# Optimization experiments

Hardware: AMD Instinct MI355X
Metric: run time of the kernel (lower is better)

## Reference

```python
import jax, jax.numpy as jnp
import numpy as np

GRID = 32  # hard-coded voxel resolution in the original module


def setup_inputs() -> dict:
    key = jax.random.key(0)
    k1, k2 = jax.random.split(key)
    points = jax.random.normal(k1, (4, 100000, 3), dtype=jnp.float32)
    features = jax.random.normal(k2, (4, 100000, 64), dtype=jnp.float32)
    return {"points": points, "features": features}


def reference(points, features):
    # points: [B, N, 3], features: [B, N, F]
    B, N, _ = points.shape
    Fdim = features.shape[-1]
    # Global (over whole tensor) min/max normalization, exactly as original
    pmin = points.min()
    pmax = points.max()
    normed = (points - pmin) / (pmax - pmin + 1e-6)  # in [0, 1)
    # torch: (normed // (1/32)).long() == floor(normed * 32)
    vox = jnp.floor(normed * GRID).astype(jnp.int32)  # [B, N, 3], values in [0, 31]
    gidx = vox[..., 0] * (GRID * GRID) + vox[..., 1] * GRID + vox[..., 2]  # [B, N]
    # Scatter-max into a zero-initialized grid (zeros init == implicit max with 0,
    # matching the original torch.zeros output_grid).
    grid = jnp.zeros((B, GRID ** 3, Fdim), dtype=features.dtype)
    batch_ids = jnp.arange(B, dtype=jnp.int32)[:, None]  # [B, 1] broadcast over N
    grid = grid.at[batch_ids, gidx].max(features)
    return grid.reshape(B, GRID, GRID, GRID, Fdim)
```

## Files before the change

### kernel.cpp

```cpp
#include <hip/hip_runtime.h>

#define GRID3 32768
#define FDIM 64

__device__ __forceinline__ unsigned int enc_f32(float f) {
    unsigned int u = __float_as_uint(f);
    return (u & 0x80000000u) ? ~u : (u | 0x80000000u);
}
__device__ __forceinline__ float dec_f32(unsigned int u) {
    u = (u & 0x80000000u) ? (u ^ 0x80000000u) : ~u;
    return __uint_as_float(u);
}

__global__ void init_ws_kernel(unsigned int* ws) {
    ws[0] = 0xFFFFFFFFu;
    ws[1] = 0u;
}

__global__ void minmax_kernel(const float* __restrict__ pts, int n,
                              unsigned int* __restrict__ ws) {
    float lmin = INFINITY, lmax = -INFINITY;
    for (int i = blockIdx.x * blockDim.x + threadIdx.x; i < n;
         i += gridDim.x * blockDim.x) {
        float v = pts[i];
        lmin = fminf(lmin, v);
        lmax = fmaxf(lmax, v);
    }
    __shared__ float smin[256], smax[256];
    smin[threadIdx.x] = lmin;
    smax[threadIdx.x] = lmax;
    __syncthreads();
    for (int s = 128; s > 0; s >>= 1) {
        if (threadIdx.x < (unsigned)s) {
            smin[threadIdx.x] = fminf(smin[threadIdx.x], smin[threadIdx.x + s]);
            smax[threadIdx.x] = fmaxf(smax[threadIdx.x], smax[threadIdx.x + s]);
        }
        __syncthreads();
    }
    if (threadIdx.x == 0) {
        atomicMin(&ws[0], enc_f32(smin[0]));
        atomicMax(&ws[1], enc_f32(smax[0]));
    }
}

__global__ void scatter_kernel(const float* __restrict__ pts,
                               const float* __restrict__ feat,
                               const unsigned int* __restrict__ ws,
                               unsigned int* __restrict__ out,
                               int ntot, int N) {
    int lane = threadIdx.x & 63;
    int p = blockIdx.x * 4 + (threadIdx.x >> 6);
    if (p >= ntot) return;

    float pmin = dec_f32(ws[0]);
    float pmax = dec_f32(ws[1]);
    float denom = pmax - pmin + 1e-6f;

    float x = pts[p * 3 + 0];
    float y = pts[p * 3 + 1];
    float z = pts[p * 3 + 2];

    int vx = (int)floorf(((x - pmin) / denom) * 32.0f);
    int vy = (int)floorf(((y - pmin) / denom) * 32.0f);
    int vz = (int)floorf(((z - pmin) / denom) * 32.0f);
    vx = min(max(vx, 0), 31);
    vy = min(max(vy, 0), 31);
    vz = min(max(vz, 0), 31);
    int gidx = vx * 1024 + vy * 32 + vz;

    int b = p / N;
    float f = feat[(size_t)p * FDIM + lane];

    if (f > 0.0f) {
        unsigned int* addr = out + ((size_t)b * GRID3 + gidx) * FDIM + lane;
        atomicMax(addr, __float_as_uint(f));
    }
}

extern "C" void kernel_launch(void* const* d_in, const int* in_sizes, int n_in,
                              void* d_out, int out_size, void* d_ws, size_t ws_size,
                              hipStream_t stream) {
    const float* pts = (const float*)d_in[0];
    const float* feat = (const float*)d_in[1];
    unsigned int* ws = (unsigned int*)d_ws;

    int npts3 = in_sizes[0];
    int ntot = npts3 / 3;
    int B = out_size / (GRID3 * FDIM);
    int N = ntot / B;

    hipLaunchKernelGGL(init_ws_kernel, dim3(1), dim3(1), 0, stream, ws);
    hipLaunchKernelGGL(minmax_kernel, dim3(512), dim3(256), 0, stream,
                       pts, npts3, ws);
    hipMemsetAsync(d_out, 0, (size_t)out_size * sizeof(float), stream);
    int blocks = (ntot + 3) / 4;
    hipLaunchKernelGGL(scatter_kernel, dim3(blocks), dim3(256), 0, stream,
                       pts, feat, ws, (unsigned int*)d_out, ntot, N);
}
```

Before: 250.7 us.

## Fuse zero-fill, min/max reduction and scatter into one cooperative kernel

```diff
diff --git a/kernel.cpp b/kernel.cpp
--- a/kernel.cpp
+++ b/kernel.cpp
@@ -1,79 +1,114 @@
 #include <hip/hip_runtime.h>
+#include <hip/hip_cooperative_groups.h>
+
+namespace cg = cooperative_groups;
 
 #define GRID3 32768
 #define FDIM 64
+#define NBLOCKS 1024
+#define NTHREADS 256
+#define MMBLOCKS 512
 
-__device__ __forceinline__ unsigned int enc_f32(float f) {
-    unsigned int u = __float_as_uint(f);
-    return (u & 0x80000000u) ? ~u : (u | 0x80000000u);
-}
-__device__ __forceinline__ float dec_f32(unsigned int u) {
-    u = (u & 0x80000000u) ? (u ^ 0x80000000u) : ~u;
-    return __uint_as_float(u);
-}
+__global__ __launch_bounds__(NTHREADS, 4)
+void fused_gridpool(const float* __restrict__ pts,
+                    const float* __restrict__ feat,
+                    unsigned int* __restrict__ out,
+                    float2* __restrict__ partials,
+                    int npts_floats,
+                    int ntot,
+                    int N,
+                    int out_floats)
+{
+    const int tid = threadIdx.x;
+    const int bid = blockIdx.x;
+    __shared__ float smin[NTHREADS];
+    __shared__ float smax[NTHREADS];
 
-__global__ void init_ws_kernel(unsigned int* ws) {
-    ws[0] = 0xFFFFFFFFu;
-    ws[1] = 0u;
-}
+    {
+        const float4 z = make_float4(0.f, 0.f, 0.f, 0.f);
+        float4* o4 = reinterpret_cast<float4*>(out);
+        const int n4 = out_floats >> 2;
+        for (int i = bid * NTHREADS + tid; i < n4; i += NBLOCKS * NTHREADS)
+            o4[i] = z;
+    }
 
-__global__ void minmax_kernel(const float* __restrict__ pts, int n,
-                              unsigned int* __restrict__ ws) {
-    float lmin = INFINITY, lmax = -INFINITY;
-    for (int i = blockIdx.x * blockDim.x + threadIdx.x; i < n;
-         i += gridDim.x * blockDim.x) {
-        float v = pts[i];
-        lmin = fminf(lmin, v);
-        lmax = fmaxf(lmax, v);
+    if (bid < MMBLOCKS) {
+        float lmin = INFINITY, lmax = -INFINITY;
+        const float4* p4 = reinterpret_cast<const float4*>(pts);
+        const int n4 = npts_floats >> 2;
+        for (int i = bid * NTHREADS + tid; i < n4; i += MMBLOCKS * NTHREADS) {
+            float4 v = p4[i];
+            lmin = fminf(lmin, fminf(fminf(v.x, v.y), fminf(v.z, v.w)));
+            lmax = fmaxf(lmax, fmaxf(fmaxf(v.x, v.y), fmaxf(v.z, v.w)));
+        }
+        for (int i = (n4 << 2) + bid * NTHREADS + tid; i < npts_floats;
+             i += MMBLOCKS * NTHREADS) {
+            float v = pts[i];
+            lmin = fminf(lmin, v);
+            lmax = fmaxf(lmax, v);
+        }
+        smin[tid] = lmin;
+        smax[tid] = lmax;
+        __syncthreads();
+        for (int s = NTHREADS / 2; s > 0; s >>= 1) {
+            if (tid < s) {
+                smin[tid] = fminf(smin[tid], smin[tid + s]);
+                smax[tid] = fmaxf(smax[tid], smax[tid + s]);
+            }
+            __syncthreads();
+        }
+        if (tid == 0) partials[bid] = make_float2(smin[0], smax[0]);
     }
-    __shared__ float smin[256], smax[256];
-    smin[threadIdx.x] = lmin;
-    smax[threadIdx.x] = lmax;
-    __syncthreads();
-    for (int s = 128; s > 0; s >>= 1) {
-        if (threadIdx.x < (unsigned)s) {
-            smin[threadIdx.x] = fminf(smin[threadIdx.x], smin[threadIdx.x + s]);
-            smax[threadIdx.x] = fmaxf(smax[threadIdx.x], smax[threadIdx.x + s]);
-        }
-        __syncthreads();
+
+    cg::this_grid().sync();
+
+    const int lane = tid & 63;
+    float rmin = INFINITY, rmax = -INFINITY;
+#pragma unroll
+    for (int j = 0; j < MMBLOCKS / 64; ++j) {
+        float2 v = partials[lane + 64 * j];
+        rmin = fminf(rmin, v.x);
+        rmax = fmaxf(rmax, v.y);
     }
-    if (threadIdx.x == 0) {
-        atomicMin(&ws[0], enc_f32(smin[0]));
-        atomicMax(&ws[1], enc_f32(smax[0]));
+#pragma unroll
+    for (int s = 32; s > 0; s >>= 1) {
+        rmin = fminf(rmin, __shfl_xor(rmin, s, 64));
+        rmax = fmaxf(rmax, __shfl_xor(rmax, s, 64));
     }
-}
+    const float pmin = rmin;
+    const float denom = rmax - rmin + 1e-6f;
 
-__global__ void scatter_kernel(const float* __restrict__ pts,
-                               const float* __restrict__ feat,
-                               const unsigned int* __restrict__ ws,
-                               unsigned int* __restrict__ out,
-                               int ntot, int N) {
-    int lane = threadIdx.x & 63;
-    int p = blockIdx.x * 4 + (threadIdx.x >> 6);
-    if (p >= ntot) return;
+    const int nwaves = NBLOCKS * (NTHREADS / 64);
+    const int wid = bid * (NTHREADS / 64) + (tid >> 6);
+    const int cnt = (ntot + nwaves - 1) / nwaves;
+    const int p0 = wid * cnt;
+    const int p1 = min(ntot, p0 + cnt);
+    if (p0 >= p1) return;
 
-    float pmin = dec_f32(ws[0]);
-    float pmax = dec_f32(ws[1]);
-    float denom = pmax - pmin + 1e-6f;
+    int b = p0 / N;
+    int nextB = (b + 1) * N;
+    const float* pp = pts + (size_t)p0 * 3;
+    const float* fp = feat + (size_t)p0 * FDIM + lane;
+    unsigned int* ob = out + (size_t)b * GRID3 * FDIM + lane;
 
-    float x = pts[p * 3 + 0];
-    float y = pts[p * 3 + 1];
-    float z = pts[p * 3 + 2];
-
-    int vx = (int)floorf(((x - pmin) / denom) * 32.0f);
-    int vy = (int)floorf(((y - pmin) / denom) * 32.0f);
-    int vz = (int)floorf(((z - pmin) / denom) * 32.0f);
-    vx = min(max(vx, 0), 31);
-    vy = min(max(vy, 0), 31);
-    vz = min(max(vz, 0), 31);
-    int gidx = vx * 1024 + vy * 32 + vz;
-
-    int b = p / N;
-    float f = feat[(size_t)p * FDIM + lane];
-
-    if (f > 0.0f) {
-        unsigned int* addr = out + ((size_t)b * GRID3 + gidx) * FDIM + lane;
-        atomicMax(addr, __float_as_uint(f));
+#pragma unroll 2
+    for (int p = p0; p < p1; ++p) {
+        if (p >= nextB) { ++b; nextB += N; ob += (size_t)GRID3 * FDIM; }
+        const float x = pp[0];
+        const float y = pp[1];
+        const float zc = pp[2];
+        pp += 3;
+        const float f = fp[0];
+        fp += FDIM;
+        int vx = (int)(((x - pmin) / denom) * 32.0f);
+        int vy = (int)(((y - pmin) / denom) * 32.0f);
+        int vz = (int)(((zc - pmin) / denom) * 32.0f);
+        vx = min(max(vx, 0), 31);
+        vy = min(max(vy, 0), 31);
+        vz = min(max(vz, 0), 31);
+        const int gidx = (vx << 10) + (vy << 5) + vz;
+        if (f > 0.0f)
+            atomicMax(ob + (size_t)gidx * FDIM, __float_as_uint(f));
     }
 }
 
@@ -82,18 +117,17 @@
                               hipStream_t stream) {
     const float* pts = (const float*)d_in[0];
     const float* feat = (const float*)d_in[1];
-    unsigned int* ws = (unsigned int*)d_ws;
+    unsigned int* out = (unsigned int*)d_out;
+    float2* partials = (float2*)d_ws;
 
     int npts3 = in_sizes[0];
     int ntot = npts3 / 3;
     int B = out_size / (GRID3 * FDIM);
     int N = ntot / B;
+    int out_floats = out_size;
 
-    hipLaunchKernelGGL(init_ws_kernel, dim3(1), dim3(1), 0, stream, ws);
-    hipLaunchKernelGGL(minmax_kernel, dim3(512), dim3(256), 0, stream,
-                       pts, npts3, ws);
-    hipMemsetAsync(d_out, 0, (size_t)out_size * sizeof(float), stream);
-    int blocks = (ntot + 3) / 4;
-    hipLaunchKernelGGL(scatter_kernel, dim3(blocks), dim3(256), 0, stream,
-                       pts, feat, ws, (unsigned int*)d_out, ntot, N);
+    void* args[] = {(void*)&pts, (void*)&feat, (void*)&out, (void*)&partials,
+                    (void*)&npts3, (void*)&ntot, (void*)&N, (void*)&out_floats};
+    hipLaunchCooperativeKernel((const void*)fused_gridpool, dim3(NBLOCKS),
+                               dim3(NTHREADS), args, 0, stream);
 }
```

Result: slower. 385.3 us (+53.7%).

## Replace atomic scatter-max with per-voxel linked lists and gather pass

Applied to the files above, without the earlier changes.

```diff
diff --git a/kernel.cpp b/kernel.cpp
--- a/kernel.cpp
+++ b/kernel.cpp
@@ -20,7 +20,15 @@
 __global__ void minmax_kernel(const float* __restrict__ pts, int n,
                               unsigned int* __restrict__ ws) {
     float lmin = INFINITY, lmax = -INFINITY;
-    for (int i = blockIdx.x * blockDim.x + threadIdx.x; i < n;
+    const float4* p4 = reinterpret_cast<const float4*>(pts);
+    const int n4 = n >> 2;
+    for (int i = blockIdx.x * blockDim.x + threadIdx.x; i < n4;
+         i += gridDim.x * blockDim.x) {
+        float4 v = p4[i];
+        lmin = fminf(lmin, fminf(fminf(v.x, v.y), fminf(v.z, v.w)));
+        lmax = fmaxf(lmax, fmaxf(fmaxf(v.x, v.y), fmaxf(v.z, v.w)));
+    }
+    for (int i = (n4 << 2) + blockIdx.x * blockDim.x + threadIdx.x; i < n;
          i += gridDim.x * blockDim.x) {
         float v = pts[i];
         lmin = fminf(lmin, v);
@@ -41,6 +49,56 @@
         atomicMin(&ws[0], enc_f32(smin[0]));
         atomicMax(&ws[1], enc_f32(smax[0]));
     }
+}
+
+__global__ void build_kernel(const float* __restrict__ pts,
+                             const unsigned int* __restrict__ ws,
+                             unsigned int* __restrict__ head,
+                             unsigned int* __restrict__ next,
+                             int ntot, int N) {
+    int i = blockIdx.x * blockDim.x + threadIdx.x;
+    if (i >= ntot) return;
+
+    float pmin = dec_f32(ws[0]);
+    float pmax = dec_f32(ws[1]);
+    float denom = pmax - pmin + 1e-6f;
+
+    float x = pts[i * 3 + 0];
+    float y = pts[i * 3 + 1];
+    float z = pts[i * 3 + 2];
+
+    int vx = (int)(((x - pmin) / denom) * 32.0f);
+    int vy = (int)(((y - pmin) / denom) * 32.0f);
+    int vz = (int)(((z - pmin) / denom) * 32.0f);
+    vx = min(max(vx, 0), 31);
+    vy = min(max(vy, 0), 31);
+    vz = min(max(vz, 0), 31);
+
+    int b = i / N;
+    int bin = b * GRID3 + (vx << 10) + (vy << 5) + vz;
+
+    unsigned int old = atomicExch(&head[bin], (unsigned int)i);
+    next[i] = old;
+}
+
+__global__ __launch_bounds__(256)
+void gather_kernel(const float* __restrict__ feat,
+                   const unsigned int* __restrict__ head,
+                   const unsigned int* __restrict__ next,
+                   float* __restrict__ out, int nbins) {
+    int bin = blockIdx.x * 4 + (threadIdx.x >> 6);
+    int lane = threadIdx.x & 63;
+    if (bin >= nbins) return;
+
+    float acc = 0.0f;
+    unsigned int p = head[bin];
+    while (p != 0xFFFFFFFFu) {
+        float f = feat[(size_t)p * FDIM + lane];
+        unsigned int np = next[p];
+        acc = fmaxf(acc, f);
+        p = np;
+    }
+    out[(size_t)bin * FDIM + lane] = acc;
 }
 
 __global__ void scatter_kernel(const float* __restrict__ pts,
@@ -70,7 +128,6 @@
 
     int b = p / N;
     float f = feat[(size_t)p * FDIM + lane];
-
     if (f > 0.0f) {
         unsigned int* addr = out + ((size_t)b * GRID3 + gidx) * FDIM + lane;
         atomicMax(addr, __float_as_uint(f));
@@ -88,12 +145,26 @@
     int ntot = npts3 / 3;
     int B = out_size / (GRID3 * FDIM);
     int N = ntot / B;
+    int nbins = B * GRID3;
+
+    size_t need = 256 + (size_t)nbins * 4 + (size_t)ntot * 4;
 
     hipLaunchKernelGGL(init_ws_kernel, dim3(1), dim3(1), 0, stream, ws);
     hipLaunchKernelGGL(minmax_kernel, dim3(512), dim3(256), 0, stream,
                        pts, npts3, ws);
-    hipMemsetAsync(d_out, 0, (size_t)out_size * sizeof(float), stream);
-    int blocks = (ntot + 3) / 4;
-    hipLaunchKernelGGL(scatter_kernel, dim3(blocks), dim3(256), 0, stream,
-                       pts, feat, ws, (unsigned int*)d_out, ntot, N);
+
+    if (ws_size >= need) {
+        unsigned int* head = ws + 64;
+        unsigned int* next = head + nbins;
+        hipMemsetAsync(head, 0xFF, (size_t)nbins * 4, stream);
+        hipLaunchKernelGGL(build_kernel, dim3((ntot + 255) / 256), dim3(256), 0,
+                           stream, pts, ws, head, next, ntot, N);
+        hipLaunchKernelGGL(gather_kernel, dim3((nbins + 3) / 4), dim3(256), 0,
+                           stream, feat, head, next, (float*)d_out, nbins);
+    } else {
+        hipMemsetAsync(d_out, 0, (size_t)out_size * sizeof(float), stream);
+        int blocks = (ntot + 3) / 4;
+        hipLaunchKernelGGL(scatter_kernel, dim3(blocks), dim3(256), 0, stream,
+                           pts, feat, ws, (unsigned int*)d_out, ntot, N);
+    }
 }
```

Result: slower. 347.6 us (+38.6%).
